# Kernel tuning notes

Hardware: AMD Instinct MI355X
Metric: run time of the kernel (lower is better)

The kernel has to match this reference:

```python
import jax, jax.numpy as jnp
import numpy as np

N, M, K, D = 100000, 8, 256, 64  # batch, n_quantizer, n_codeword, len_subvec
LEN_VEC = M * D


def setup_inputs() -> dict:
    key = jax.random.key(0)
    k1, k2 = jax.random.split(key)
    x = jax.random.normal(k1, (N, LEN_VEC), dtype=jnp.float32)
    codebooks = jax.random.normal(k2, (M, K, D), dtype=jnp.float32)
    return {"x": x, "codebooks": codebooks, "soft_rate": -1}


def reference(x, codebooks, soft_rate):
    # x: [N, len_vec] -> [N, M, D] subvectors
    xs = x.reshape(x.shape[0], M, D)
    # squared L2 distances per (sample, quantizer, codeword): [N, M, K]
    x_sq = jnp.sum(xs * xs, axis=-1, keepdims=True)            # [N, M, 1]
    c_sq = jnp.sum(codebooks * codebooks, axis=-1)             # [M, K]
    cross = jnp.einsum('nmd,mkd->nmk', xs, codebooks)          # [N, M, K]
    dist = x_sq - 2.0 * cross + c_sq[None, :, :]               # [N, M, K]
    ids = jnp.argmin(dist, axis=-1)                            # [N, M]
    if soft_rate > 0:
        # soft assignment: convex combo of codewords weighted by softmax(-soft_rate * dist)
        w = jax.nn.softmax(-soft_rate * dist, axis=-1)         # [N, M, K]
        q = jnp.einsum('nmk,mkd->nmd', w, codebooks)           # [N, M, D]
    else:
        # hard assignment: gather nearest codeword per quantizer
        q = jnp.take_along_axis(codebooks[None], ids[:, :, None, None], axis=2)
        q = q[:, :, 0, :]                                      # [N, M, D]
    Q_x = q.reshape(-1, LEN_VEC)                               # [N, len_vec]
    id_x = ids.T.astype(jnp.int64)                             # [M, N], matches torch layout
    return Q_x, id_x
```

## Files before the change

### kernel.cpp

```cpp
#include <hip/hip_runtime.h>

#define NN 100000
#define MM 8
#define KK 256
#define DD 64
#define BROWS 128
#define NTILES ((NN + BROWS - 1) / BROWS)

typedef _Float16 half8 __attribute__((ext_vector_type(8)));
typedef float    f32x4 __attribute__((ext_vector_type(4)));


__global__ __launch_bounds__(256) void pq_prep_kernel(
    const float* __restrict__ cb, half8* __restrict__ whi,
    half8* __restrict__ wlo, float* __restrict__ csq)
{
    const int t = blockIdx.x * 256 + threadIdx.x;
    const int m = t >> 11, rest = t & 2047;
    const int c = rest >> 8, k = rest & 255;
    const float* src = cb + ((size_t)(m * KK + k)) * DD + c * 8;
    half8 h, l;
#pragma unroll
    for (int j = 0; j < 8; ++j) {
        float v = src[j];
        _Float16 hi = (_Float16)v;
        h[j] = hi;
        l[j] = (_Float16)((v - (float)hi) * 2048.0f);
    }
    whi[t] = h;
    wlo[t] = l;

    if (t < MM * KK) {
        const float* cr = cb + (size_t)t * DD;
        float s0 = 0.f, s1 = 0.f, s2 = 0.f, s3 = 0.f;
#pragma unroll
        for (int d = 0; d < DD; d += 4) {
            s0 = fmaf(cr[d + 0], cr[d + 0], s0);
            s1 = fmaf(cr[d + 1], cr[d + 1], s1);
            s2 = fmaf(cr[d + 2], cr[d + 2], s2);
            s3 = fmaf(cr[d + 3], cr[d + 3], s3);
        }
        csq[t] = (s0 + s1) + (s2 + s3);
    }
}

#define DELTA 4.0e-3f

__global__ __launch_bounds__(256, 2) void pq_main_kernel(
    const float* __restrict__ x, const half8* __restrict__ whi,
    const half8* __restrict__ wlo, const float* __restrict__ csqg,
    const float* __restrict__ cbf, float* __restrict__ qout,
    float* __restrict__ idout)
{
    __shared__ half8 Bh[8][128];
    __shared__ half8 Bl[8][128];
    __shared__ float csq_s[KK];
    __shared__ int   cand_k[BROWS];

    const int m   = blockIdx.y;
    const int n0  = blockIdx.x * BROWS;
    const int tid = threadIdx.x;
    const int w = tid >> 6, L = tid & 63;
    const int q = L >> 4, ci = L & 15;

    csq_s[tid] = csqg[m * KK + tid];

    half8 Ah[2][2], Al[2][2];
#pragma unroll
    for (int rb = 0; rb < 2; ++rb) {
        int n = n0 + w * 32 + rb * 16 + ci;
        if (n > NN - 1) n = NN - 1;
        const float4* xp = (const float4*)(x + (size_t)n * (MM * DD) + m * DD);
#pragma unroll
        for (int t = 0; t < 2; ++t) {
            float4 v0 = xp[t * 8 + q * 2 + 0];
            float4 v1 = xp[t * 8 + q * 2 + 1];
            float vs[8] = {v0.x, v0.y, v0.z, v0.w, v1.x, v1.y, v1.z, v1.w};
#pragma unroll
            for (int j = 0; j < 8; ++j) {
                _Float16 hi = (_Float16)vs[j];
                Ah[rb][t][j] = hi;
                Al[rb][t][j] = (_Float16)((vs[j] - (float)hi) * 2048.0f);
            }
        }
    }

    float d1v[2][4], d2v[2][4];
    int   k1v[2][4];
#pragma unroll
    for (int rb = 0; rb < 2; ++rb)
#pragma unroll
        for (int r = 0; r < 4; ++r) { d1v[rb][r] = 3.4e38f; d2v[rb][r] = 3.4e38f; k1v[rb][r] = 0; }

    const half8* wh_m = whi + m * 2048;
    const half8* wl_m = wlo + m * 2048;

    for (int kh = 0; kh < 2; ++kh) {
        __syncthreads();
        for (int idx = tid; idx < 1024; idx += 256) {
            int c = idx >> 7, kl = idx & 127;
            Bh[c][kl] = wh_m[c * 256 + kh * 128 + kl];
            Bl[c][kl] = wl_m[c * 256 + kh * 128 + kl];
        }
        __syncthreads();

        for (int sc = 0; sc < 2; ++sc) {
            f32x4 acc1[2][4], acc2[2][4];
            const f32x4 z = {0.f, 0.f, 0.f, 0.f};
#pragma unroll
            for (int rb = 0; rb < 2; ++rb)
#pragma unroll
                for (int s = 0; s < 4; ++s) { acc1[rb][s] = z; acc2[rb][s] = z; }

#pragma unroll
            for (int sl = 0; sl < 4; ++sl) {
                const int kloc = (sc * 4 + sl) * 16 + ci;
                half8 bh0 = Bh[0 + q][kloc];
                half8 bh1 = Bh[4 + q][kloc];
                half8 bl0 = Bl[0 + q][kloc];
                half8 bl1 = Bl[4 + q][kloc];
#pragma unroll
                for (int rb = 0; rb < 2; ++rb) {
                    acc1[rb][sl] = __builtin_amdgcn_mfma_f32_16x16x32_f16(Ah[rb][0], bh0, acc1[rb][sl], 0, 0, 0);
                    acc1[rb][sl] = __builtin_amdgcn_mfma_f32_16x16x32_f16(Ah[rb][1], bh1, acc1[rb][sl], 0, 0, 0);
                    acc2[rb][sl] = __builtin_amdgcn_mfma_f32_16x16x32_f16(Ah[rb][0], bl0, acc2[rb][sl], 0, 0, 0);
                    acc2[rb][sl] = __builtin_amdgcn_mfma_f32_16x16x32_f16(Ah[rb][1], bl1, acc2[rb][sl], 0, 0, 0);
                    acc2[rb][sl] = __builtin_amdgcn_mfma_f32_16x16x32_f16(Al[rb][0], bh0, acc2[rb][sl], 0, 0, 0);
                    acc2[rb][sl] = __builtin_amdgcn_mfma_f32_16x16x32_f16(Al[rb][1], bh1, acc2[rb][sl], 0, 0, 0);
                }
            }
#pragma unroll
            for (int sl = 0; sl < 4; ++sl) {
                const int k = kh * 128 + (sc * 4 + sl) * 16 + ci;
                const float cq = csq_s[k];
#pragma unroll
                for (int rb = 0; rb < 2; ++rb)
#pragma unroll
                    for (int r = 0; r < 4; ++r) {
                        float cross = acc1[rb][sl][r] + acc2[rb][sl][r] * (1.0f / 2048.0f);
                        float d = cq - 2.0f * cross;
                        if (d < d1v[rb][r]) {
                            d2v[rb][r] = d1v[rb][r];
                            d1v[rb][r] = d; k1v[rb][r] = k;
                        } else if (d < d2v[rb][r]) {
                            d2v[rb][r] = d;
                        }
                    }
            }
        }
    }

#pragma unroll
    for (int rb = 0; rb < 2; ++rb)
#pragma unroll
        for (int r = 0; r < 4; ++r) {
            float d = d1v[rb][r];
            int   k = k1v[rb][r];
            for (int mask = 1; mask < 16; mask <<= 1) {
                float ds = __shfl_xor(d, mask);
                int   ks = __shfl_xor(k, mask);
                if (ds < d || (ds == d && ks < k)) { d = ds; k = ks; }
            }
            const float thr = d + DELTA;
            int cnt = (d1v[rb][r] <= thr ? 1 : 0) + (d2v[rb][r] <= thr ? 1 : 0);
            for (int mask = 1; mask < 16; mask <<= 1) cnt += __shfl_xor(cnt, mask);

            const int n = n0 + w * 32 + rb * 16 + q * 4 + r;
            if (cnt > 1 && n < NN) {
                const float* xr = x + (size_t)n * (MM * DD) + m * DD;
                float s0 = 0.f, s1 = 0.f, s2 = 0.f, s3 = 0.f;
                for (int dd = 0; dd < DD; dd += 4) {
                    s0 = fmaf(xr[dd + 0], xr[dd + 0], s0);
                    s1 = fmaf(xr[dd + 1], xr[dd + 1], s1);
                    s2 = fmaf(xr[dd + 2], xr[dd + 2], s2);
                    s3 = fmaf(xr[dd + 3], xr[dd + 3], s3);
                }
                const float xsq = (s0 + s1) + (s2 + s3);
                float bd = 3.4e38f; int bk = 0;
                for (int j = 0; j < 16; ++j) {
                    const int kk = ci + 16 * j;
                    const float* c0 = cbf + ((size_t)(m * KK + kk)) * DD;
                    float a0 = 0.f, a1 = 0.f;
                    for (int dd = 0; dd < DD; dd += 2) {
                        a0 = fmaf(c0[dd + 0], xr[dd + 0], a0);
                        a1 = fmaf(c0[dd + 1], xr[dd + 1], a1);
                    }
                    const float dist = (xsq - 2.f * (a0 + a1)) + csq_s[kk];
                    if (dist < bd) { bd = dist; bk = kk; }
                }
                for (int mask = 1; mask < 16; mask <<= 1) {
                    float db = __shfl_xor(bd, mask);
                    int   kb = __shfl_xor(bk, mask);
                    if (db < bd || (db == bd && kb < bk)) { bd = db; bk = kb; }
                }
                k = bk;
            }
            if (ci == r) cand_k[w * 32 + rb * 16 + q * 4 + r] = k;
        }
    __syncthreads();

    if (tid < BROWS) {
        int n = n0 + tid;
        if (n < NN) idout[(size_t)m * NN + n] = (float)cand_k[tid];
    }
    for (int i = 0; i < 8; ++i) {
        int row = i * 16 + (tid >> 4);
        int n = n0 + row;
        if (n < NN) {
            int k = cand_k[row];
            int j = tid & 15;
            float4 v = ((const float4*)cbf)[(m * KK + k) * 16 + j];
            ((float4*)(qout + (size_t)n * (MM * DD) + m * DD))[j] = v;
        }
    }
}

extern "C" void kernel_launch(void* const* d_in, const int* in_sizes, int n_in,
                              void* d_out, int out_size, void* d_ws, size_t ws_size,
                              hipStream_t stream)
{
    const float* x  = (const float*)d_in[0];
    const float* cb = (const float*)d_in[1];

    float* qout  = (float*)d_out;
    float* idout = qout + (size_t)NN * (MM * DD);

    half8* whi = (half8*)d_ws;
    half8* wlo = (half8*)((char*)d_ws + 256 * 1024);
    float* csq = (float*)((char*)d_ws + 512 * 1024);

    pq_prep_kernel<<<dim3(64), dim3(256), 0, stream>>>(cb, whi, wlo, csq);

    pq_main_kernel<<<dim3(NTILES, MM), dim3(256), 0, stream>>>(
        x, whi, wlo, csq, cb, qout, idout);
}
```

Baseline: 442.1 us.

## Stream codebook fragments from global memory with register prefetch instead of LDS staging

Drops the shared-memory staging of the fp16 hi/lo codebook tiles. Each lane now loads its B fragments directly from global memory (L2-resident), with a one-step register prefetch of the next 16-codeword slice. The loop is restructured into 16 iterations with smaller accumulator sets, and launch bounds rise to 4 blocks per SIMD to lift occupancy. This removes LDS traffic and two barriers per half, but adds redundant global/L2 loads across waves and tighter register pressure.

```diff
diff --git a/kernel.cpp b/kernel.cpp
--- a/kernel.cpp
+++ b/kernel.cpp
@@ -46,14 +46,12 @@
 
 #define DELTA 4.0e-3f
 
-__global__ __launch_bounds__(256, 2) void pq_main_kernel(
+__global__ __launch_bounds__(256, 4) void pq_main_kernel(
     const float* __restrict__ x, const half8* __restrict__ whi,
     const half8* __restrict__ wlo, const float* __restrict__ csqg,
     const float* __restrict__ cbf, float* __restrict__ qout,
     float* __restrict__ idout)
 {
-    __shared__ half8 Bh[8][128];
-    __shared__ half8 Bl[8][128];
     __shared__ float csq_s[KK];
     __shared__ int   cand_k[BROWS];
 
@@ -92,62 +90,50 @@
 #pragma unroll
         for (int r = 0; r < 4; ++r) { d1v[rb][r] = 3.4e38f; d2v[rb][r] = 3.4e38f; k1v[rb][r] = 0; }
 
-    const half8* wh_m = whi + m * 2048;
-    const half8* wl_m = wlo + m * 2048;
-
-    for (int kh = 0; kh < 2; ++kh) {
-        __syncthreads();
-        for (int idx = tid; idx < 1024; idx += 256) {
-            int c = idx >> 7, kl = idx & 127;
-            Bh[c][kl] = wh_m[c * 256 + kh * 128 + kl];
-            Bl[c][kl] = wl_m[c * 256 + kh * 128 + kl];
-        }
-        __syncthreads();
-
-        for (int sc = 0; sc < 2; ++sc) {
-            f32x4 acc1[2][4], acc2[2][4];
-            const f32x4 z = {0.f, 0.f, 0.f, 0.f};
-#pragma unroll
-            for (int rb = 0; rb < 2; ++rb)
-#pragma unroll
-                for (int s = 0; s < 4; ++s) { acc1[rb][s] = z; acc2[rb][s] = z; }
-
-#pragma unroll
-            for (int sl = 0; sl < 4; ++sl) {
-                const int kloc = (sc * 4 + sl) * 16 + ci;
-                half8 bh0 = Bh[0 + q][kloc];
-                half8 bh1 = Bh[4 + q][kloc];
-                half8 bl0 = Bl[0 + q][kloc];
-                half8 bl1 = Bl[4 + q][kloc];
-#pragma unroll
-                for (int rb = 0; rb < 2; ++rb) {
-                    acc1[rb][sl] = __builtin_amdgcn_mfma_f32_16x16x32_f16(Ah[rb][0], bh0, acc1[rb][sl], 0, 0, 0);
-                    acc1[rb][sl] = __builtin_amdgcn_mfma_f32_16x16x32_f16(Ah[rb][1], bh1, acc1[rb][sl], 0, 0, 0);
-                    acc2[rb][sl] = __builtin_amdgcn_mfma_f32_16x16x32_f16(Ah[rb][0], bl0, acc2[rb][sl], 0, 0, 0);
-                    acc2[rb][sl] = __builtin_amdgcn_mfma_f32_16x16x32_f16(Ah[rb][1], bl1, acc2[rb][sl], 0, 0, 0);
-                    acc2[rb][sl] = __builtin_amdgcn_mfma_f32_16x16x32_f16(Al[rb][0], bh0, acc2[rb][sl], 0, 0, 0);
-                    acc2[rb][sl] = __builtin_amdgcn_mfma_f32_16x16x32_f16(Al[rb][1], bh1, acc2[rb][sl], 0, 0, 0);
-                }
-            }
-#pragma unroll
-            for (int sl = 0; sl < 4; ++sl) {
-                const int k = kh * 128 + (sc * 4 + sl) * 16 + ci;
-                const float cq = csq_s[k];
-#pragma unroll
-                for (int rb = 0; rb < 2; ++rb)
-#pragma unroll
-                    for (int r = 0; r < 4; ++r) {
-                        float cross = acc1[rb][sl][r] + acc2[rb][sl][r] * (1.0f / 2048.0f);
-                        float d = cq - 2.0f * cross;
-                        if (d < d1v[rb][r]) {
-                            d2v[rb][r] = d1v[rb][r];
-                            d1v[rb][r] = d; k1v[rb][r] = k;
-                        } else if (d < d2v[rb][r]) {
-                            d2v[rb][r] = d;
-                        }
-                    }
-            }
-        }
+    const half8* bh0p = whi + m * 2048 + q * 256;
+    const half8* bh1p = whi + m * 2048 + (4 + q) * 256;
+    const half8* bl0p = wlo + m * 2048 + q * 256;
+    const half8* bl1p = wlo + m * 2048 + (4 + q) * 256;
+
+    __syncthreads();
+
+    half8 bh0 = bh0p[ci], bh1 = bh1p[ci], bl0 = bl0p[ci], bl1 = bl1p[ci];
+
+    for (int kt = 0; kt < 16; ++kt) {
+        int kn = kt + 1; if (kn > 15) kn = 15;
+        const int o = kn * 16 + ci;
+        half8 nh0 = bh0p[o], nh1 = bh1p[o], nl0 = bl0p[o], nl1 = bl1p[o];
+
+        f32x4 acc1[2], acc2[2];
+        const f32x4 z = {0.f, 0.f, 0.f, 0.f};
+        acc1[0] = z; acc1[1] = z; acc2[0] = z; acc2[1] = z;
+#pragma unroll
+        for (int rb = 0; rb < 2; ++rb) {
+            acc1[rb] = __builtin_amdgcn_mfma_f32_16x16x32_f16(Ah[rb][0], bh0, acc1[rb], 0, 0, 0);
+            acc1[rb] = __builtin_amdgcn_mfma_f32_16x16x32_f16(Ah[rb][1], bh1, acc1[rb], 0, 0, 0);
+            acc2[rb] = __builtin_amdgcn_mfma_f32_16x16x32_f16(Ah[rb][0], bl0, acc2[rb], 0, 0, 0);
+            acc2[rb] = __builtin_amdgcn_mfma_f32_16x16x32_f16(Ah[rb][1], bl1, acc2[rb], 0, 0, 0);
+            acc2[rb] = __builtin_amdgcn_mfma_f32_16x16x32_f16(Al[rb][0], bh0, acc2[rb], 0, 0, 0);
+            acc2[rb] = __builtin_amdgcn_mfma_f32_16x16x32_f16(Al[rb][1], bh1, acc2[rb], 0, 0, 0);
+        }
+
+        const int k = kt * 16 + ci;
+        const float cq = csq_s[k];
+#pragma unroll
+        for (int rb = 0; rb < 2; ++rb)
+#pragma unroll
+            for (int r = 0; r < 4; ++r) {
+                float cross = acc1[rb][r] + acc2[rb][r] * (1.0f / 2048.0f);
+                float d = cq - 2.0f * cross;
+                if (d < d1v[rb][r]) {
+                    d2v[rb][r] = d1v[rb][r];
+                    d1v[rb][r] = d; k1v[rb][r] = k;
+                } else if (d < d2v[rb][r]) {
+                    d2v[rb][r] = d;
+                }
+            }
+
+        bh0 = nh0; bh1 = nh1; bl0 = nl0; bl1 = nl1;
     }
 
 #pragma unroll
```

New measurement: 424.3 us. 4.0% less time.
